# Performance work log

Measured on AMD Instinct MI355X. Metric: run time of the kernel, lower is better.

The kernel has to match this reference:

```python
import jax, jax.numpy as jnp
import numpy as np
import math

NUM_WORDS = 8192
WORD_WIDTH = 512
PROJ_WIDTH = 64
NUM_HEADS = 8
SCALE_FACTOR = 100.0

def setup_inputs() -> dict:
    key = jax.random.key(0)
    kx, kq, kk, kv, ko = jax.random.split(key, 5)
    x = jax.random.normal(kx, (NUM_WORDS, WORD_WIDTH), dtype=jnp.float32)
    w_q = jax.random.normal(kq, (WORD_WIDTH, PROJ_WIDTH), dtype=jnp.float32) / SCALE_FACTOR
    w_k = jax.random.normal(kk, (WORD_WIDTH, PROJ_WIDTH), dtype=jnp.float32) / SCALE_FACTOR
    w_v = jax.random.normal(kv, (WORD_WIDTH, PROJ_WIDTH), dtype=jnp.float32) / SCALE_FACTOR
    w_o = jax.random.normal(ko, (WORD_WIDTH, WORD_WIDTH), dtype=jnp.float32)
    return {"x": x, "w_q": w_q, "w_k": w_k, "w_v": w_v, "w_o": w_o}

def reference(x, w_q, w_k, w_v, w_o):
    # Single self-attention head (all 8 heads in the source share the same weights).
    q = x @ w_q            # [N, P]
    k = x @ w_k            # [N, P]
    v = x @ w_v            # [N, P]
    scores = jax.nn.softmax((q @ k.T) / jnp.sqrt(jnp.float32(q.shape[1])), axis=1)  # [N, N]
    head = scores @ v      # [N, P]
    # concat of NUM_HEADS identical head outputs along dim=1
    concat = jnp.tile(head, (1, NUM_HEADS))  # [N, NUM_HEADS*P]
    return concat @ w_o    # [N, WORD_WIDTH]
```

## Files before the change

### kernel.cpp

```cpp
#include <hip/hip_runtime.h>
#include <stdint.h>

#define N_WORDS 8192
#define LOG2E_8 0.18033688011112043f

typedef __attribute__((ext_vector_type(8))) short short8;
typedef __attribute__((ext_vector_type(4))) float f32x4;
typedef __attribute__((ext_vector_type(4))) _Float16 half4;

__device__ __forceinline__ unsigned short f32_to_bf16(float f) {
    union { float f; unsigned u; } v; v.f = f;
    unsigned u = v.u;
    return (unsigned short)((u + 0x7FFFu + ((u >> 16) & 1u)) >> 16);
}

__device__ __forceinline__ unsigned short f32_to_f16(float f) {
    union { _Float16 h; unsigned short u; } cv;
    cv.h = (_Float16)f;
    return cv.u;
}

__device__ __forceinline__ void async16(const void* g, void* l) {
    __builtin_amdgcn_global_load_lds(
        (const __attribute__((address_space(1))) unsigned int*)g,
        (__attribute__((address_space(3))) unsigned int*)l, 16, 0, 0);
}

__global__ __launch_bounds__(256) void xcvt_kernel(
    const float* __restrict__ x, unsigned short* __restrict__ xb)
{
    int ci = blockIdx.x * 256 + threadIdx.x;
    int row = ci >> 6, c = ci & 63;
    const float* src = x + ((size_t)row * 512 + c * 8);
    float4 v0 = *(const float4*)(src);
    float4 v1 = *(const float4*)(src + 4);
    unsigned u0 = f32_to_bf16(v0.x) | ((unsigned)f32_to_bf16(v0.y) << 16);
    unsigned u1 = f32_to_bf16(v0.z) | ((unsigned)f32_to_bf16(v0.w) << 16);
    unsigned u2 = f32_to_bf16(v1.x) | ((unsigned)f32_to_bf16(v1.y) << 16);
    unsigned u3 = f32_to_bf16(v1.z) | ((unsigned)f32_to_bf16(v1.w) << 16);
    int dst = (c & ~7) | ((c ^ (row & 7)) & 7);
    *(uint4*)(xb + (size_t)row * 512 + dst * 8) = make_uint4(u0, u1, u2, u3);
}

__global__ __launch_bounds__(192) void wprep_kernel(
    const float* __restrict__ wq, const float* __restrict__ wk,
    const float* __restrict__ wv, unsigned short* __restrict__ wT)
{
    int n = threadIdx.x;
    int c = blockIdx.x;
    const float* w = (n < 64) ? wq : (n < 128) ? wk : wv;
    int col = n & 63;
    float scale = (n < 64) ? LOG2E_8 : 1.0f;
    unsigned short o[8];
#pragma unroll
    for (int j = 0; j < 8; ++j)
        o[j] = f32_to_bf16(w[(size_t)(c * 8 + j) * 64 + col] * scale);
    unsigned u0 = o[0] | ((unsigned)o[1] << 16);
    unsigned u1 = o[2] | ((unsigned)o[3] << 16);
    unsigned u2 = o[4] | ((unsigned)o[5] << 16);
    unsigned u3 = o[6] | ((unsigned)o[7] << 16);
    int dst = (c & ~7) | ((c ^ (n & 7)) & 7);
    *(uint4*)(wT + (size_t)n * 512 + dst * 8) = make_uint4(u0, u1, u2, u3);
}

__global__ __launch_bounds__(256) void woeff_kernel(
    const float* __restrict__ wo, float* __restrict__ we)
{
    int i = blockIdx.x * 256 + threadIdx.x;
    int p = i >> 9;
    int j = i & 511;
    float s = 0.0f;
#pragma unroll
    for (int h = 0; h < 8; ++h) s += wo[(size_t)(h * 64 + p) * 512 + j];
    we[i] = s;
}

__global__ __launch_bounds__(256) void qkv_gemm(
    const unsigned short* __restrict__ xb,
    const unsigned short* __restrict__ wT,
    unsigned short* __restrict__ qB, unsigned short* __restrict__ kB,
    unsigned short* __restrict__ vH)
{
    __shared__ __align__(16) unsigned short ldsX[2][16 * 64];
    __shared__ __align__(16) unsigned short ldsW[2][192 * 64];

    int t = threadIdx.x;
    int wvid = t >> 6, lane = t & 63;
    int lq = lane & 15, quad = lane >> 4;
    int m0 = blockIdx.x * 16;

    f32x4 acc[3];
#pragma unroll
    for (int v = 0; v < 3; ++v) acc[v] = (f32x4){0.f, 0.f, 0.f, 0.f};

    auto stage = [&](int kb, int buf) {
        int k0 = kb * 64;
        if (wvid < 2) {
            int L = wvid * 64 + lane;
            int row = m0 + (L >> 3), ct = L & 7;
            const char* src = (const char*)xb + ((size_t)row * 512 + k0) * 2 + ct * 16;
            async16(src, (char*)(&ldsX[buf][0]) + (size_t)(wvid * 64) * 16);
        }
#pragma unroll
        for (int i = 0; i < 6; ++i) {
            int L0 = (i * 4 + wvid) * 64;
            int L = L0 + lane;
            int n = L >> 3, ct = L & 7;
            const char* src = (const char*)wT + ((size_t)n * 512 + k0) * 2 + ct * 16;
            async16(src, (char*)(&ldsW[buf][0]) + (size_t)L0 * 16);
        }
    };

    stage(0, 0);
    for (int kb = 0; kb < 8; ++kb) {
        __syncthreads();
        if (kb < 7) stage(kb + 1, (kb + 1) & 1);
        const unsigned short* Xb = &ldsX[kb & 1][0];
        const unsigned short* Wb = &ldsW[kb & 1][0];
        int s7m = lq & 7;
        short8 a0 = *(const short8*)(Xb + lq * 64 + ((quad ^ s7m) << 3));
        short8 a1 = *(const short8*)(Xb + lq * 64 + (((4 + quad) ^ s7m) << 3));
#pragma unroll
        for (int v = 0; v < 3; ++v) {
            int n = (wvid * 3 + v) * 16 + lq;
            const unsigned short* wr = Wb + n * 64;
            int s7 = n & 7;
            short8 b0 = *(const short8*)(wr + ((quad ^ s7) << 3));
            short8 b1 = *(const short8*)(wr + (((4 + quad) ^ s7) << 3));
            acc[v] = __builtin_amdgcn_mfma_f32_16x16x32_bf16(a0, b0, acc[v], 0, 0, 0);
            acc[v] = __builtin_amdgcn_mfma_f32_16x16x32_bf16(a1, b1, acc[v], 0, 0, 0);
        }
    }

#pragma unroll
    for (int v = 0; v < 3; ++v) {
        int n = (wvid * 3 + v) * 16 + lq;
#pragma unroll
        for (int r = 0; r < 4; ++r) {
            int row = m0 + quad * 4 + r;
            float val = acc[v][r];
            if (n < 64) {
                int col = ((((n >> 3) ^ (row & 7)) << 3)) | (n & 7);
                qB[(size_t)row * 64 + col] = f32_to_bf16(val);
            } else if (n < 128) {
                int c = n - 64;
                int col = ((((c >> 3) ^ (row & 7)) << 3)) | (c & 7);
                kB[(size_t)row * 64 + col] = f32_to_bf16(val);
            } else {
                int c = n - 128;
                int rs = (row & ~63) | (((((row >> 3) & 7) ^ (c & 7)) << 3)) | (row & 7);
                vH[(size_t)c * N_WORDS + rs] = f32_to_f16(val);
            }
        }
    }
}

__global__ __launch_bounds__(256) void attn_kernel(
    const unsigned short* __restrict__ qB,
    const unsigned short* __restrict__ kB,
    const unsigned short* __restrict__ vH,
    float* __restrict__ pO, float* __restrict__ pl, int nk)
{
    __shared__ __align__(16) unsigned short ldsK[2][64 * 64];
    __shared__ __align__(16) unsigned short ldsV[2][64 * 64];

    int t = threadIdx.x;
    int wvid = t >> 6, lane = t & 63;
    int lq = lane & 15, quad = lane >> 4;
    int mbase = blockIdx.x * 128 + wvid * 32;
    int n0 = blockIdx.y * nk;

    short8 qf[2][2];
#pragma unroll
    for (int qs = 0; qs < 2; ++qs) {
        int row = mbase + qs * 16 + lq;
        const unsigned short* qr = qB + (size_t)row * 64;
        int s7 = row & 7;
        qf[qs][0] = *(const short8*)(qr + ((quad ^ s7) << 3));
        qf[qs][1] = *(const short8*)(qr + (((4 + quad) ^ s7) << 3));
    }

    f32x4 oacc[2][4];
#pragma unroll
    for (int qs = 0; qs < 2; ++qs)
#pragma unroll
        for (int vt = 0; vt < 4; ++vt) oacc[qs][vt] = (f32x4){0.f, 0.f, 0.f, 0.f};
    float lsum0 = 0.f, lsum1 = 0.f;

    auto stage = [&](int tile, int buf) {
        int nb = n0 + tile * 64;
        const char* gK = (const char*)kB + (size_t)nb * 128;
#pragma unroll
        for (int i = 0; i < 2; ++i) {
            int L0 = (wvid * 2 + i) * 64;
            async16(gK + (size_t)(L0 + lane) * 16, (char*)(&ldsK[buf][0]) + (size_t)L0 * 16);
        }
#pragma unroll
        for (int i = 0; i < 2; ++i) {
            int L0 = (wvid * 2 + i) * 64;
            int L = L0 + lane;
            int vcol = L >> 3, ct = L & 7;
            const char* src = (const char*)vH + (size_t)vcol * 16384 + (size_t)nb * 2 + ct * 16;
            async16(src, (char*)(&ldsV[buf][0]) + (size_t)L0 * 16);
        }
    };

    int tiles = nk >> 6;
    stage(0, 0);
    for (int tt = 0; tt < tiles; ++tt) {
        __syncthreads();
        if (tt + 1 < tiles) stage(tt + 1, (tt + 1) & 1);
        const unsigned short* Kb = &ldsK[tt & 1][0];
        const unsigned short* Vb = &ldsV[tt & 1][0];

#pragma unroll
        for (int nt = 0; nt < 4; ++nt) {
            int s7 = lq & 7;
            const unsigned short* kr = Kb + (nt * 16 + lq) * 64;
            short8 a0 = *(const short8*)(kr + ((quad ^ s7) << 3));
            short8 a1 = *(const short8*)(kr + (((4 + quad) ^ s7) << 3));
            f32x4 st0 = (f32x4){0.f, 0.f, 0.f, 0.f};
            f32x4 st1 = (f32x4){0.f, 0.f, 0.f, 0.f};
            st0 = __builtin_amdgcn_mfma_f32_16x16x32_bf16(a0, qf[0][0], st0, 0, 0, 0);
            st0 = __builtin_amdgcn_mfma_f32_16x16x32_bf16(a1, qf[0][1], st0, 0, 0, 0);
            st1 = __builtin_amdgcn_mfma_f32_16x16x32_bf16(a0, qf[1][0], st1, 0, 0, 0);
            st1 = __builtin_amdgcn_mfma_f32_16x16x32_bf16(a1, qf[1][1], st1, 0, 0, 0);

            half4 p0, p1;
#pragma unroll
            for (int r = 0; r < 4; ++r) {
                float e = exp2f(st0[r]);
                lsum0 += e;
                p0[r] = (_Float16)e;
            }
#pragma unroll
            for (int r = 0; r < 4; ++r) {
                float e = exp2f(st1[r]);
                lsum1 += e;
                p1[r] = (_Float16)e;
            }

            int j2 = nt * 2 + (quad >> 1);
            int off = (quad & 1) * 4;
#pragma unroll
            for (int vt = 0; vt < 4; ++vt) {
                int vcol = vt * 16 + lq;
                int p = j2 ^ (vcol & 7);
                half4 vb = *(const half4*)(Vb + vcol * 64 + (p << 3) + off);
                oacc[0][vt] = __builtin_amdgcn_mfma_f32_16x16x16f16(p0, vb, oacc[0][vt], 0, 0, 0);
                oacc[1][vt] = __builtin_amdgcn_mfma_f32_16x16x16f16(p1, vb, oacc[1][vt], 0, 0, 0);
            }
        }
    }

    lsum0 += __shfl_xor(lsum0, 16); lsum0 += __shfl_xor(lsum0, 32);
    lsum1 += __shfl_xor(lsum1, 16); lsum1 += __shfl_xor(lsum1, 32);

    size_t obase = (size_t)blockIdx.y * N_WORDS;
    if (quad == 0) {
        pl[obase + mbase + lq] = lsum0;
        pl[obase + mbase + 16 + lq] = lsum1;
    }
#pragma unroll
    for (int qs = 0; qs < 2; ++qs)
#pragma unroll
        for (int vt = 0; vt < 4; ++vt)
#pragma unroll
            for (int r = 0; r < 4; ++r) {
                int row = mbase + qs * 16 + quad * 4 + r;
                pO[(obase + row) * 64 + vt * 16 + lq] = oacc[qs][vt][r];
            }
}

__global__ __launch_bounds__(256) void out_kernel(
    const float* __restrict__ pO, const float* __restrict__ pl,
    const float* __restrict__ we, float* __restrict__ out, int S)
{
    __shared__ __align__(16) float ldsHT[64 * 16];
    __shared__ float ldsL[16];
    int t = threadIdx.x;
    int r0 = blockIdx.x * 16;
    int r = t >> 4, c4 = (t & 15) * 4;

    float4 a = make_float4(0.f, 0.f, 0.f, 0.f);
    for (int s = 0; s < S; ++s) {
        float4 pv = *(const float4*)(pO + ((size_t)s * N_WORDS + r0 + r) * 64 + c4);
        a.x += pv.x; a.y += pv.y; a.z += pv.z; a.w += pv.w;
    }
    if (t < 16) {
        float lr = 0.f;
        for (int s = 0; s < S; ++s) lr += pl[(size_t)s * N_WORDS + r0 + t];
        ldsL[t] = lr;
    }
    __syncthreads();
    float inv = 1.0f / ldsL[r];
    ldsHT[(c4 + 0) * 16 + r] = a.x * inv;
    ldsHT[(c4 + 1) * 16 + r] = a.y * inv;
    ldsHT[(c4 + 2) * 16 + r] = a.z * inv;
    ldsHT[(c4 + 3) * 16 + r] = a.w * inv;
    __syncthreads();

    int w = t >> 6, l = t & 63;
    int cg = w & 1, rg = w >> 1;
    int j0 = cg * 256 + l * 4;

    float4 acc[8];
#pragma unroll
    for (int rr = 0; rr < 8; ++rr) acc[rr] = make_float4(0.f, 0.f, 0.f, 0.f);

    for (int k = 0; k < 64; ++k) {
        float4 wv = *(const float4*)(we + (size_t)k * 512 + j0);
        float4 h0 = *(const float4*)(ldsHT + k * 16 + rg * 8);
        float4 h1 = *(const float4*)(ldsHT + k * 16 + rg * 8 + 4);
        float hr[8] = {h0.x, h0.y, h0.z, h0.w, h1.x, h1.y, h1.z, h1.w};
#pragma unroll
        for (int rr = 0; rr < 8; ++rr) {
            acc[rr].x = fmaf(hr[rr], wv.x, acc[rr].x);
            acc[rr].y = fmaf(hr[rr], wv.y, acc[rr].y);
            acc[rr].z = fmaf(hr[rr], wv.z, acc[rr].z);
            acc[rr].w = fmaf(hr[rr], wv.w, acc[rr].w);
        }
    }

#pragma unroll
    for (int rr = 0; rr < 8; ++rr) {
        int row = r0 + rg * 8 + rr;
        *(float4*)(out + (size_t)row * 512 + j0) = acc[rr];
    }
}

extern "C" void kernel_launch(void* const* d_in, const int* in_sizes, int n_in,
                              void* d_out, int out_size, void* d_ws, size_t ws_size,
                              hipStream_t stream)
{
    const float* x  = (const float*)d_in[0];
    const float* wq = (const float*)d_in[1];
    const float* wk = (const float*)d_in[2];
    const float* wv = (const float*)d_in[3];
    const float* wo = (const float*)d_in[4];
    float* out = (float*)d_out;

    char* ws = (char*)d_ws;
    unsigned short* xb = (unsigned short*)(ws);
    unsigned short* wT = (unsigned short*)(ws + 8388608);
    float* we = (float*)(ws + 8585216);
    float* pl = (float*)(ws + 8716288);
    unsigned short* qB = (unsigned short*)(ws + 8978432);
    unsigned short* kB = (unsigned short*)(ws + 10027008);
    unsigned short* vH = (unsigned short*)(ws + 11075584);
    float* pO = (float*)(ws + 12124160);

    int S = (ws_size >= (size_t)12124160 + 8u * 2097152u) ? 8 : 4;
    int nk = N_WORDS / S;

    hipLaunchKernelGGL(xcvt_kernel, dim3(2048), dim3(256), 0, stream, x, xb);
    hipLaunchKernelGGL(wprep_kernel, dim3(64), dim3(192), 0, stream, wq, wk, wv, wT);
    hipLaunchKernelGGL(woeff_kernel, dim3(128), dim3(256), 0, stream, wo, we);
    hipLaunchKernelGGL(qkv_gemm, dim3(512), dim3(256), 0, stream, xb, wT, qB, kB, vH);
    hipLaunchKernelGGL(attn_kernel, dim3(64, S), dim3(256), 0, stream,
                       qB, kB, vH, pO, pl, nk);
    hipLaunchKernelGGL(out_kernel, dim3(512), dim3(256), 0, stream,
                       pO, pl, we, out, S);
}
```

Measured before the change: 137.6 us.

## Fuse x bf16 conversion into QKV GEMM, merge weight prep kernels, raise split-K

Removes the separate x-to-bf16 conversion kernel: the QKV GEMM now async-loads fp32 x tiles into LDS with an XOR swizzle and converts them to bf16 in registers before the MFMAs. The GEMM tile grows from 16 to 32 rows, so each weight fragment feeds two MFMAs and half as many blocks are launched. The weight-transpose and W_o head-sum kernels are merged into one launch. The attention key-split count rises from 8 to 16 when workspace allows, using the space freed by dropping the bf16 x buffer. The trade-offs are doubled LDS for x, fp32 reads of x in the GEMM, and more partial outputs for the final reduction.

```diff
diff --git a/kernel.cpp b/kernel.cpp
--- a/kernel.cpp
+++ b/kernel.cpp
@@ -26,80 +26,77 @@
         (__attribute__((address_space(3))) unsigned int*)l, 16, 0, 0);
 }
 
-__global__ __launch_bounds__(256) void xcvt_kernel(
-    const float* __restrict__ x, unsigned short* __restrict__ xb)
-{
-    int ci = blockIdx.x * 256 + threadIdx.x;
-    int row = ci >> 6, c = ci & 63;
-    const float* src = x + ((size_t)row * 512 + c * 8);
-    float4 v0 = *(const float4*)(src);
-    float4 v1 = *(const float4*)(src + 4);
-    unsigned u0 = f32_to_bf16(v0.x) | ((unsigned)f32_to_bf16(v0.y) << 16);
-    unsigned u1 = f32_to_bf16(v0.z) | ((unsigned)f32_to_bf16(v0.w) << 16);
-    unsigned u2 = f32_to_bf16(v1.x) | ((unsigned)f32_to_bf16(v1.y) << 16);
-    unsigned u3 = f32_to_bf16(v1.z) | ((unsigned)f32_to_bf16(v1.w) << 16);
-    int dst = (c & ~7) | ((c ^ (row & 7)) & 7);
-    *(uint4*)(xb + (size_t)row * 512 + dst * 8) = make_uint4(u0, u1, u2, u3);
-}
-
-__global__ __launch_bounds__(192) void wprep_kernel(
+__device__ __forceinline__ short8 pack_bf16x8(float4 a, float4 b) {
+    short8 r;
+    r[0] = (short)f32_to_bf16(a.x); r[1] = (short)f32_to_bf16(a.y);
+    r[2] = (short)f32_to_bf16(a.z); r[3] = (short)f32_to_bf16(a.w);
+    r[4] = (short)f32_to_bf16(b.x); r[5] = (short)f32_to_bf16(b.y);
+    r[6] = (short)f32_to_bf16(b.z); r[7] = (short)f32_to_bf16(b.w);
+    return r;
+}
+
+__global__ __launch_bounds__(256) void prep_kernel(
     const float* __restrict__ wq, const float* __restrict__ wk,
-    const float* __restrict__ wv, unsigned short* __restrict__ wT)
-{
-    int n = threadIdx.x;
-    int c = blockIdx.x;
-    const float* w = (n < 64) ? wq : (n < 128) ? wk : wv;
-    int col = n & 63;
-    float scale = (n < 64) ? LOG2E_8 : 1.0f;
-    unsigned short o[8];
-#pragma unroll
-    for (int j = 0; j < 8; ++j)
-        o[j] = f32_to_bf16(w[(size_t)(c * 8 + j) * 64 + col] * scale);
-    unsigned u0 = o[0] | ((unsigned)o[1] << 16);
-    unsigned u1 = o[2] | ((unsigned)o[3] << 16);
-    unsigned u2 = o[4] | ((unsigned)o[5] << 16);
-    unsigned u3 = o[6] | ((unsigned)o[7] << 16);
-    int dst = (c & ~7) | ((c ^ (n & 7)) & 7);
-    *(uint4*)(wT + (size_t)n * 512 + dst * 8) = make_uint4(u0, u1, u2, u3);
-}
-
-__global__ __launch_bounds__(256) void woeff_kernel(
-    const float* __restrict__ wo, float* __restrict__ we)
-{
-    int i = blockIdx.x * 256 + threadIdx.x;
-    int p = i >> 9;
-    int j = i & 511;
-    float s = 0.0f;
-#pragma unroll
-    for (int h = 0; h < 8; ++h) s += wo[(size_t)(h * 64 + p) * 512 + j];
-    we[i] = s;
+    const float* __restrict__ wv, const float* __restrict__ wo,
+    unsigned short* __restrict__ wT, float* __restrict__ we)
+{
+    int b = blockIdx.x, t = threadIdx.x;
+    if (b < 48) {
+        int job = b * 256 + t;
+        int n = job >> 6, c = job & 63;
+        const float* w = (n < 64) ? wq : (n < 128) ? wk : wv;
+        int col = n & 63;
+        float scale = (n < 64) ? LOG2E_8 : 1.0f;
+        unsigned short o[8];
+#pragma unroll
+        for (int j = 0; j < 8; ++j)
+            o[j] = f32_to_bf16(w[(size_t)(c * 8 + j) * 64 + col] * scale);
+        unsigned u0 = o[0] | ((unsigned)o[1] << 16);
+        unsigned u1 = o[2] | ((unsigned)o[3] << 16);
+        unsigned u2 = o[4] | ((unsigned)o[5] << 16);
+        unsigned u3 = o[6] | ((unsigned)o[7] << 16);
+        int dst = (c & ~7) | ((c ^ (n & 7)) & 7);
+        *(uint4*)(wT + (size_t)n * 512 + dst * 8) = make_uint4(u0, u1, u2, u3);
+    } else {
+        int i = (b - 48) * 256 + t;
+        int p = i >> 9, j = i & 511;
+        float s = 0.0f;
+#pragma unroll
+        for (int h = 0; h < 8; ++h) s += wo[(size_t)(h * 64 + p) * 512 + j];
+        we[i] = s;
+    }
 }
 
 __global__ __launch_bounds__(256) void qkv_gemm(
-    const unsigned short* __restrict__ xb,
+    const float* __restrict__ x,
     const unsigned short* __restrict__ wT,
     unsigned short* __restrict__ qB, unsigned short* __restrict__ kB,
     unsigned short* __restrict__ vH)
 {
-    __shared__ __align__(16) unsigned short ldsX[2][16 * 64];
+    __shared__ __align__(16) float ldsX[2][32 * 64];
     __shared__ __align__(16) unsigned short ldsW[2][192 * 64];
 
     int t = threadIdx.x;
     int wvid = t >> 6, lane = t & 63;
     int lq = lane & 15, quad = lane >> 4;
-    int m0 = blockIdx.x * 16;
-
-    f32x4 acc[3];
-#pragma unroll
-    for (int v = 0; v < 3; ++v) acc[v] = (f32x4){0.f, 0.f, 0.f, 0.f};
+    int m0 = blockIdx.x * 32;
+
+    f32x4 acc[3][2];
+#pragma unroll
+    for (int v = 0; v < 3; ++v)
+#pragma unroll
+        for (int qs = 0; qs < 2; ++qs) acc[v][qs] = (f32x4){0.f, 0.f, 0.f, 0.f};
 
     auto stage = [&](int kb, int buf) {
         int k0 = kb * 64;
-        if (wvid < 2) {
-            int L = wvid * 64 + lane;
-            int row = m0 + (L >> 3), ct = L & 7;
-            const char* src = (const char*)xb + ((size_t)row * 512 + k0) * 2 + ct * 16;
-            async16(src, (char*)(&ldsX[buf][0]) + (size_t)(wvid * 64) * 16);
+#pragma unroll
+        for (int i = 0; i < 2; ++i) {
+            int L0 = (wvid * 2 + i) * 64;
+            int L = L0 + lane;
+            int row = L >> 4, cslot = L & 15;
+            int cg = (cslot & 8) | ((cslot ^ (row & 7)) & 7);
+            const char* src = (const char*)(x + (size_t)(m0 + row) * 512 + k0) + cg * 16;
+            async16(src, (char*)(&ldsX[buf][0]) + (size_t)L0 * 16);
         }
 #pragma unroll
         for (int i = 0; i < 6; ++i) {
@@ -115,20 +112,34 @@
     for (int kb = 0; kb < 8; ++kb) {
         __syncthreads();
         if (kb < 7) stage(kb + 1, (kb + 1) & 1);
-        const unsigned short* Xb = &ldsX[kb & 1][0];
+        const float4* Xb = (const float4*)(&ldsX[kb & 1][0]);
         const unsigned short* Wb = &ldsW[kb & 1][0];
-        int s7m = lq & 7;
-        short8 a0 = *(const short8*)(Xb + lq * 64 + ((quad ^ s7m) << 3));
-        short8 a1 = *(const short8*)(Xb + lq * 64 + (((4 + quad) ^ s7m) << 3));
+        int s7 = lq & 7;
+
+        short8 af[2][2];
+#pragma unroll
+        for (int qs = 0; qs < 2; ++qs) {
+            int lr = qs * 16 + lq;
+            int c0 = (2 * quad) ^ s7;
+            float4 x0 = Xb[lr * 16 + c0];
+            float4 x1 = Xb[lr * 16 + (c0 ^ 1)];
+            float4 x2 = Xb[lr * 16 + (8 | c0)];
+            float4 x3 = Xb[lr * 16 + ((8 | c0) ^ 1)];
+            af[qs][0] = pack_bf16x8(x0, x1);
+            af[qs][1] = pack_bf16x8(x2, x3);
+        }
 #pragma unroll
         for (int v = 0; v < 3; ++v) {
             int n = (wvid * 3 + v) * 16 + lq;
             const unsigned short* wr = Wb + n * 64;
-            int s7 = n & 7;
-            short8 b0 = *(const short8*)(wr + ((quad ^ s7) << 3));
-            short8 b1 = *(const short8*)(wr + (((4 + quad) ^ s7) << 3));
-            acc[v] = __builtin_amdgcn_mfma_f32_16x16x32_bf16(a0, b0, acc[v], 0, 0, 0);
-            acc[v] = __builtin_amdgcn_mfma_f32_16x16x32_bf16(a1, b1, acc[v], 0, 0, 0);
+            int s7n = n & 7;
+            short8 b0 = *(const short8*)(wr + ((quad ^ s7n) << 3));
+            short8 b1 = *(const short8*)(wr + (((4 + quad) ^ s7n) << 3));
+#pragma unroll
+            for (int qs = 0; qs < 2; ++qs) {
+                acc[v][qs] = __builtin_amdgcn_mfma_f32_16x16x32_bf16(af[qs][0], b0, acc[v][qs], 0, 0, 0);
+                acc[v][qs] = __builtin_amdgcn_mfma_f32_16x16x32_bf16(af[qs][1], b1, acc[v][qs], 0, 0, 0);
+            }
         }
     }
 
@@ -136,22 +147,24 @@
     for (int v = 0; v < 3; ++v) {
         int n = (wvid * 3 + v) * 16 + lq;
 #pragma unroll
-        for (int r = 0; r < 4; ++r) {
-            int row = m0 + quad * 4 + r;
-            float val = acc[v][r];
-            if (n < 64) {
-                int col = ((((n >> 3) ^ (row & 7)) << 3)) | (n & 7);
-                qB[(size_t)row * 64 + col] = f32_to_bf16(val);
-            } else if (n < 128) {
-                int c = n - 64;
-                int col = ((((c >> 3) ^ (row & 7)) << 3)) | (c & 7);
-                kB[(size_t)row * 64 + col] = f32_to_bf16(val);
-            } else {
-                int c = n - 128;
-                int rs = (row & ~63) | (((((row >> 3) & 7) ^ (c & 7)) << 3)) | (row & 7);
-                vH[(size_t)c * N_WORDS + rs] = f32_to_f16(val);
-            }
-        }
+        for (int qs = 0; qs < 2; ++qs)
+#pragma unroll
+            for (int r = 0; r < 4; ++r) {
+                int row = m0 + qs * 16 + quad * 4 + r;
+                float val = acc[v][qs][r];
+                if (n < 64) {
+                    int col = ((((n >> 3) ^ (row & 7)) << 3)) | (n & 7);
+                    qB[(size_t)row * 64 + col] = f32_to_bf16(val);
+                } else if (n < 128) {
+                    int c = n - 64;
+                    int col = ((((c >> 3) ^ (row & 7)) << 3)) | (c & 7);
+                    kB[(size_t)row * 64 + col] = f32_to_bf16(val);
+                } else {
+                    int c = n - 128;
+                    int rs = (row & ~63) | (((((row >> 3) & 7) ^ (c & 7)) << 3)) | (row & 7);
+                    vH[(size_t)c * N_WORDS + rs] = f32_to_f16(val);
+                }
+            }
     }
 }
 
@@ -341,22 +354,21 @@
     float* out = (float*)d_out;
 
     char* ws = (char*)d_ws;
-    unsigned short* xb = (unsigned short*)(ws);
-    unsigned short* wT = (unsigned short*)(ws + 8388608);
-    float* we = (float*)(ws + 8585216);
-    float* pl = (float*)(ws + 8716288);
-    unsigned short* qB = (unsigned short*)(ws + 8978432);
-    unsigned short* kB = (unsigned short*)(ws + 10027008);
-    unsigned short* vH = (unsigned short*)(ws + 11075584);
-    float* pO = (float*)(ws + 12124160);
-
-    int S = (ws_size >= (size_t)12124160 + 8u * 2097152u) ? 8 : 4;
+    unsigned short* wT = (unsigned short*)(ws);
+    float* we = (float*)(ws + 196608);
+    float* pl = (float*)(ws + 327680);
+    unsigned short* qB = (unsigned short*)(ws + 851968);
+    unsigned short* kB = (unsigned short*)(ws + 1900544);
+    unsigned short* vH = (unsigned short*)(ws + 2949120);
+    float* pO = (float*)(ws + 3997696);
+
+    int S = (ws_size >= (size_t)3997696 + 16u * 2097152u) ? 16 : 8;
     int nk = N_WORDS / S;
 
-    hipLaunchKernelGGL(xcvt_kernel, dim3(2048), dim3(256), 0, stream, x, xb);
-    hipLaunchKernelGGL(wprep_kernel, dim3(64), dim3(192), 0, stream, wq, wk, wv, wT);
-    hipLaunchKernelGGL(woeff_kernel, dim3(128), dim3(256), 0, stream, wo, we);
-    hipLaunchKernelGGL(qkv_gemm, dim3(512), dim3(256), 0, stream, xb, wT, qB, kB, vH);
+    hipLaunchKernelGGL(prep_kernel, dim3(176), dim3(256), 0, stream,
+                       wq, wk, wv, wo, wT, we);
+    hipLaunchKernelGGL(qkv_gemm, dim3(256), dim3(256), 0, stream,
+                       x, wT, qB, kB, vH);
     hipLaunchKernelGGL(attn_kernel, dim3(64, S), dim3(256), 0, stream,
                        qB, kB, vH, pO, pl, nk);
     hipLaunchKernelGGL(out_kernel, dim3(512), dim3(256), 0, stream,
```

Measured after the change: 137.2 us. Within noise of the previous version (-0.2%).
